# Kernel optimization log

Measured on AMD Instinct MI355X. Metric: run time of the kernel, lower is better.

Reference implementation:

```python
import jax, jax.numpy as jnp
import numpy as np

B, N, T, D, H, K = 16, 64, 32, 512, 256, 13
S = N * T  # flattened document length
PAD_TAG = 0


def setup_inputs():
    key = jax.random.key(0)
    ks = jax.random.split(key, 16)
    x = jax.random.normal(ks[0], (B, N, T, D), jnp.float32)
    x_gcn = jax.random.normal(ks[1], (B, N, D), jnp.float32)
    length = jax.random.randint(ks[2], (B, N), 1, T + 1)
    mask = (jnp.arange(T)[None, None, :] < length[:, :, None]).astype(jnp.int32)
    tags = jax.random.randint(ks[3], (B, N, T), 0, K)
    s = 0.05
    w_ih_f = jax.random.normal(ks[4], (4 * H, D), jnp.float32) * s
    w_hh_f = jax.random.normal(ks[5], (4 * H, H), jnp.float32) * s
    b_f = jax.random.normal(ks[6], (4 * H,), jnp.float32) * s
    w_ih_b = jax.random.normal(ks[7], (4 * H, D), jnp.float32) * s
    w_hh_b = jax.random.normal(ks[8], (4 * H, H), jnp.float32) * s
    b_b = jax.random.normal(ks[9], (4 * H,), jnp.float32) * s
    mlp_w = jax.random.normal(ks[10], (K, 2 * H), jnp.float32) * s
    mlp_b = jax.random.normal(ks[11], (K,), jnp.float32) * s
    transitions = jax.random.normal(ks[12], (K, K), jnp.float32) * s
    start_trans = jax.random.normal(ks[13], (K,), jnp.float32) * s
    end_trans = jax.random.normal(ks[14], (K,), jnp.float32) * s
    return dict(x=x, x_gcn=x_gcn, mask=mask, length=length, tags=tags,
                w_ih_f=w_ih_f, w_hh_f=w_hh_f, b_f=b_f,
                w_ih_b=w_ih_b, w_hh_b=w_hh_b, b_b=b_b,
                mlp_w=mlp_w, mlp_b=mlp_b,
                transitions=transitions, start_trans=start_trans, end_trans=end_trans)


def _pack_one(v, dest):
    # scatter valid rows to compacted positions; invalid rows land in dummy slot S
    out = jnp.zeros((S + 1,) + v.shape[1:], v.dtype).at[dest].set(v)
    return out[:S]


def union_layer(x, x_gcn, mask, length, tags):
    xf = x.reshape(B, S, D)
    mf = mask.reshape(B, S)
    tf = tags.reshape(B, S)
    doc_len = length.sum(-1)  # (B,)
    cum = jnp.cumsum(mf, axis=1)
    dest = jnp.where(mf == 1, cum - 1, S)  # invalid -> dummy slot
    new_x = jax.vmap(_pack_one)(xf, dest)
    new_tag = jax.vmap(_pack_one)(tf, dest)  # pad tag = 0
    new_mask = (jnp.arange(S)[None, :] < doc_len[:, None]).astype(mf.dtype)
    gcn_flat = jnp.broadcast_to(x_gcn[:, :, None, :], (B, N, T, D)).reshape(B, S, D)
    return gcn_flat + new_x, new_mask, doc_len, new_tag


def lstm_dir(xs, w_ih, w_hh, b):
    # xs: (B, S, Din) -> hidden states (B, S, H)
    def step(carry, xt):
        h, c = carry
        g = xt @ w_ih.T + h @ w_hh.T + b
        i, f, gg, o = jnp.split(g, 4, axis=-1)
        c = jax.nn.sigmoid(f) * c + jax.nn.sigmoid(i) * jnp.tanh(gg)
        h = jax.nn.sigmoid(o) * jnp.tanh(c)
        return (h, c), h
    init = (jnp.zeros((B, H), xs.dtype), jnp.zeros((B, H), xs.dtype))
    _, hs = jax.lax.scan(step, init, jnp.swapaxes(xs, 0, 1))
    return jnp.swapaxes(hs, 0, 1)


def bilstm(new_x, doc_len, w_ih_f, w_hh_f, b_f, w_ih_b, w_hh_b, b_b):
    t = jnp.arange(S)[None, :]
    L = doc_len[:, None]
    rev = jnp.where(t < L, L - 1 - t, t)  # per-sample reversal within valid region (involution)
    out_f = lstm_dir(new_x, w_ih_f, w_hh_f, b_f)
    x_rev = jnp.take_along_axis(new_x, rev[:, :, None], axis=1)
    out_b = lstm_dir(x_rev, w_ih_b, w_hh_b, b_b)
    out_b = jnp.take_along_axis(out_b, rev[:, :, None], axis=1)
    return jnp.concatenate([out_f, out_b], axis=-1)  # (B, S, 2H)


def crf_log_likelihood(logits, tags, mask, doc_len, transitions, start_trans, end_trans):
    maskf = mask.astype(logits.dtype)
    # numerator: score of the gold path
    emit = jnp.take_along_axis(logits, tags[:, :, None], axis=2)[..., 0]  # (B,S)
    num = start_trans[tags[:, 0]] + (emit * maskf).sum(1)
    tr = transitions[tags[:, :-1], tags[:, 1:]] * maskf[:, 1:]
    num = num + tr.sum(1)
    last_tag = jnp.take_along_axis(tags, (doc_len - 1)[:, None], axis=1)[:, 0]
    num = num + end_trans[last_tag]
    # denominator: forward algorithm
    alpha0 = start_trans[None, :] + logits[:, 0]
    def step(alpha, inp):
        e, m = inp  # (B,K), (B,)
        new = jax.nn.logsumexp(alpha[:, :, None] + transitions[None] + e[:, None, :], axis=1)
        return jnp.where(m[:, None] > 0, new, alpha), None
    alpha, _ = jax.lax.scan(step, alpha0,
                            (jnp.swapaxes(logits[:, 1:], 0, 1), jnp.swapaxes(mask[:, 1:], 0, 1)))
    log_z = jax.nn.logsumexp(alpha + end_trans[None, :], axis=-1)
    return num - log_z  # (B,) per-doc log-likelihood (keepdim=True)


def reference(x, x_gcn, mask, length, tags,
              w_ih_f, w_hh_f, b_f, w_ih_b, w_hh_b, b_b,
              mlp_w, mlp_b, transitions, start_trans, end_trans):
    new_x, new_mask, doc_len, new_tag = union_layer(x, x_gcn, mask, length, tags)
    out = bilstm(new_x, doc_len, w_ih_f, w_hh_f, b_f, w_ih_b, w_hh_b, b_b)
    out = out * new_mask[:, :, None].astype(out.dtype)  # packed-seq padding semantics
    logits = out @ mlp_w.T + mlp_b  # (B, S, K)
    ll = crf_log_likelihood(logits, new_tag, new_mask, doc_len,
                            transitions, start_trans, end_trans)
    return logits, new_mask, ll
```

## Files before the change

### kernel.cpp

```cpp
#include <hip/hip_runtime.h>
#include <hip/hip_fp16.h>
#include <hip/hip_bf16.h>

#define B_ 16
#define N_ 64
#define T_ 32
#define D_ 512
#define H_ 256
#define K_ 13
#define S_ 2048
#define G4_ 1024

typedef float f32x4 __attribute__((ext_vector_type(4)));
typedef short s16x8 __attribute__((ext_vector_type(8)));
typedef int   i32x4 __attribute__((ext_vector_type(4)));

#define LOG2E 1.44269504f
#define INVQ  2.0505324e-5f
#define INVQ2 2.9582873e-5f

#define BAR() do { \
  asm volatile("s_waitcnt lgkmcnt(0)" ::: "memory"); \
  __builtin_amdgcn_s_barrier(); \
  __builtin_amdgcn_sched_barrier(0); \
} while (0)

__device__ __forceinline__ float sigm(float x){ return 1.0f/(1.0f+__expf(-x)); }
__device__ __forceinline__ float tanh_fast(float x){ return 1.0f - 2.0f/(1.0f+__expf(2.0f*x)); }

__device__ __forceinline__ float sigm2(float y){ return __builtin_amdgcn_rcpf(1.0f + exp2f(-y)); }
__device__ __forceinline__ float tanh2(float y){ return 1.0f - 2.0f*__builtin_amdgcn_rcpf(1.0f + exp2f(2.0f*y)); }

__global__ void k_prep(const int* __restrict__ length, int* __restrict__ cum, int* __restrict__ doc){
  const int b = threadIdx.x >> 6, n = threadIdx.x & 63;
  const int v = length[b*N_ + n];
  int x = v;
  #pragma unroll
  for (int d = 1; d < 64; d <<= 1){
    int y = __shfl_up(x, d);
    if (n >= d) x += y;
  }
  cum[b*N_ + n] = x - v;
  if (n == 63) doc[b] = x;
}

__global__ __launch_bounds__(256) void k_cast(const float* __restrict__ wf, const float* __restrict__ wb,
                       const float* __restrict__ hf, const float* __restrict__ hb,
                       ushort* __restrict__ wih, signed char* __restrict__ whh8){
  const int i = blockIdx.x*256 + threadIdx.x;
  if (i < 2*G4_*D_){
    const int dir = i / (G4_*D_); const int r = i % (G4_*D_);
    const float v = dir ? wb[r] : wf[r];
    ((__hip_bfloat16*)wih)[i] = __float2bfloat16(v);
  } else {
    const int j2 = i - 2*G4_*D_;
    if (j2 < 2*G4_*H_){
      const int dir = j2 >> 18; const int r = j2 & 262143;
      const float v = (dir ? hb : hf)[r];
      int q = (int)rintf(v * 384.0f);
      whh8[j2] = (signed char)min(127, max(-127, q));
    }
  }
}

__global__ __launch_bounds__(256) void k_srcmap(const int* __restrict__ length, const int* __restrict__ cum,
                         const int* __restrict__ tags, int* __restrict__ src, int* __restrict__ ntag){
  const int i = blockIdx.x*256 + threadIdx.x;
  const int b = i >> 11, nt = i & 2047, n = nt >> 5, t = nt & 31;
  if (t < length[b*N_ + n]){
    const int dest = cum[b*N_ + n] + t;
    src[b*S_ + dest] = nt;
    ntag[b*S_ + dest] = tags[i];
  }
}

__global__ __launch_bounds__(256) void k_newx(const float* __restrict__ x, const float* __restrict__ gcn,
                      const int* __restrict__ src, const int* __restrict__ doc,
                      ushort* __restrict__ nx, float* __restrict__ mask_out){
  const int r = blockIdx.x; const int b = r >> 11, s = r & 2047;
  const int L = doc[b];
  const int d = threadIdx.x*2;
  const float2 g2 = *(const float2*)&gcn[((size_t)(b*N_ + (s>>5)))*D_ + d];
  float v0 = g2.x, v1 = g2.y;
  if (s < L){
    const int nt = src[r];
    const float2 x2 = *(const float2*)&x[((size_t)(b*S_ + nt))*D_ + d];
    v0 += x2.x; v1 += x2.y;
  }
  __hip_bfloat16* o = (__hip_bfloat16*)nx + (size_t)r*D_ + d;
  o[0] = __float2bfloat16(v0); o[1] = __float2bfloat16(v1);
  if (threadIdx.x == 0) mask_out[r] = (s < L) ? 1.0f : 0.0f;
}

__global__ __launch_bounds__(256) void k_gemm(const ushort* __restrict__ A, const ushort* __restrict__ Bw,
    const float* __restrict__ bias_f, const float* __restrict__ bias_b,
    const int* __restrict__ doc, __half* __restrict__ pre){
  const int m0 = blockIdx.x*128, n0 = blockIdx.y*128;
  const int b = m0 >> 11, s0 = m0 & 2047;
  if (s0 >= doc[b]) return;
  __shared__ __align__(16) ushort la[128*40];
  __shared__ __align__(16) ushort lb[128*40];
  const int tid = threadIdx.x, lane = tid & 63, w = tid >> 6;
  const int wr = w >> 1, wc = w & 1;
  const int fr = lane & 15, fq = lane >> 4;
  f32x4 acc[4][4] = {};
  const int srow = tid >> 1;
  const int sko  = (tid & 1)*16;
  for (int kt = 0; kt < 16; ++kt){
    const int k0 = kt*32;
    const float4 a0 = *(const float4*)&A[(size_t)(m0+srow)*512 + k0 + sko];
    const float4 a1 = *(const float4*)&A[(size_t)(m0+srow)*512 + k0 + sko + 8];
    const float4 b0 = *(const float4*)&Bw[(size_t)(n0+srow)*512 + k0 + sko];
    const float4 b1 = *(const float4*)&Bw[(size_t)(n0+srow)*512 + k0 + sko + 8];
    *(float4*)&la[srow*40 + sko]     = a0;
    *(float4*)&la[srow*40 + sko + 8] = a1;
    *(float4*)&lb[srow*40 + sko]     = b0;
    *(float4*)&lb[srow*40 + sko + 8] = b1;
    __syncthreads();
    s16x8 af[4], bfr[4];
    #pragma unroll
    for (int mi=0; mi<4; ++mi) af[mi] = *(const s16x8*)&la[(wr*64+mi*16+fr)*40 + fq*8];
    #pragma unroll
    for (int ni=0; ni<4; ++ni) bfr[ni] = *(const s16x8*)&lb[(wc*64+ni*16+fr)*40 + fq*8];
    #pragma unroll
    for (int mi=0; mi<4; ++mi){
      #pragma unroll
      for (int ni=0; ni<4; ++ni){
        acc[mi][ni] = __builtin_amdgcn_mfma_f32_16x16x32_bf16(af[mi], bfr[ni], acc[mi][ni], 0, 0, 0);
      }
    }
    __syncthreads();
  }
  #pragma unroll
  for (int ni=0; ni<4; ++ni){
    const int n = n0 + wc*64 + ni*16 + fr;
    const float bv = (n < 1024) ? bias_f[n] : bias_b[n-1024];
    const int dir = n >> 10, g = (n >> 8) & 3, u = n & 255;
    const int col = dir*1024 + u*4 + g;
    #pragma unroll
    for (int mi=0; mi<4; ++mi){
      const int mb = m0 + wr*64 + mi*16 + fq*4;
      #pragma unroll
      for (int j=0; j<4; ++j)
        pre[(size_t)(mb+j)*2048 + col] = __float2half((acc[mi][ni][j] + bv)*LOG2E);
    }
  }
}

__global__ __launch_bounds__(512, 2) void k_recur12(
    const signed char* __restrict__ W8,
    const __half* __restrict__ pre, const int* __restrict__ doc,
    __half* __restrict__ outh)
{
  const int b = blockIdx.x >> 1, dir = blockIdx.x & 1;
  const int tid = threadIdx.x, lane = tid & 63, wv = tid >> 6;
  const int L = doc[b];

  __shared__ __align__(16) signed char hq[2][256];

  if (tid < 128) ((unsigned*)hq)[tid] = 0u;

  i32x4 wfrag[2][4][4];
  #pragma unroll
  for (int nt = 0; nt < 2; ++nt)
    #pragma unroll
    for (int g = 0; g < 4; ++g){
      const int row = g*256 + wv*32 + nt*16 + (lane & 15);
      #pragma unroll
      for (int kt = 0; kt < 4; ++kt)
        wfrag[nt][g][kt] = *(const i32x4*)&W8[(size_t)dir*262144 + (size_t)row*256 + kt*64 + (lane>>4)*16];
    }

  const int u = wv*32 + (lane & 31);
  const int koff = (lane >> 4)*16;
  const int pos0 = dir ? (L-1) : 0;
  const __half* pp = pre + ((size_t)(b*S_ + pos0))*2048 + dir*1024 + u*4;
  __half*       op = outh + ((size_t)(b*S_ + pos0))*512 + dir*256 + u;
  const ptrdiff_t dp  = dir ? -2048 : 2048;
  const ptrdiff_t dph = dir ? -512  : 512;

  float cst = 0.f;
  uint2 pv, pvn = {0,0};
  pv = *(const uint2*)pp;
  const i32x4 z = {0,0,0,0};
  BAR();

  for (int t = 0; t < L; ++t){
    if (t+1 < L) pvn = *(const uint2*)(pp + dp);
    pp += dp;

    const int rbuf = (t+1) & 1, wbuf = t & 1;

    i32x4 af[4];
    #pragma unroll
    for (int kt = 0; kt < 4; ++kt)
      af[kt] = *(const i32x4*)&hq[rbuf][kt*64 + koff];

    auto chain4 = [&](const i32x4* w4) -> int {
      i32x4 a = __builtin_amdgcn_mfma_i32_16x16x64_i8(af[0], w4[0], z, 0, 0, 0);
      a = __builtin_amdgcn_mfma_i32_16x16x64_i8(af[1], w4[1], a, 0, 0, 0);
      a = __builtin_amdgcn_mfma_i32_16x16x64_i8(af[2], w4[2], a, 0, 0, 0);
      a = __builtin_amdgcn_mfma_i32_16x16x64_i8(af[3], w4[3], a, 0, 0, 0);
      return a[0];
    };

    const bool hi = (lane & 16) != 0;
    const __half2* ph = (const __half2*)&pv;
    const float2 p01 = __half22float2(ph[0]);
    const float2 p23 = __half22float2(ph[1]);

    const int i0 = chain4(wfrag[0][0]), i1 = chain4(wfrag[1][0]);
    const int f0 = chain4(wfrag[0][1]), f1 = chain4(wfrag[1][1]);
    const int q0 = chain4(wfrag[0][2]), q1 = chain4(wfrag[1][2]);
    const float giy = (float)(hi ? i1 : i0)*INVQ2 + p01.x;
    const float gfy = (float)(hi ? f1 : f0)*INVQ2 + p01.y;
    const float ggy = (float)(hi ? q1 : q0)*INVQ2 + p23.x;
    const int o0 = chain4(wfrag[0][3]), o1 = chain4(wfrag[1][3]);
    const float c = sigm2(gfy)*cst + sigm2(giy)*tanh2(ggy);
    cst = c;
    const float goy = (float)(hi ? o1 : o0)*INVQ2 + p23.y;
    const float hval = sigm2(goy)*tanh2(c*LOG2E);

    if (lane < 32){
      *op = __float2half(hval);
      hq[wbuf][u] = (signed char)(int)rintf(hval*127.0f);
    }
    op += dph;
    pv = pvn;
    BAR();
  }
}

__global__ __launch_bounds__(256) void k_logits(const __half* __restrict__ outh, const float* __restrict__ mw,
    const float* __restrict__ mb, const int* __restrict__ doc, float* __restrict__ logits){
  const int w = threadIdx.x >> 6, lane = threadIdx.x & 63;
  const int r = blockIdx.x*4 + w;
  const int b = r >> 11, s = r & 2047;
  if (s >= doc[b]){
    if (lane < 13) logits[(size_t)r*13 + lane] = mb[lane];
    return;
  }
  float xv[8];
  #pragma unroll
  for (int m=0; m<8; ++m) xv[m] = __half2float(outh[(size_t)r*512 + lane + m*64]);
  #pragma unroll
  for (int k=0; k<13; ++k){
    float p = 0.f;
    #pragma unroll
    for (int m=0; m<8; ++m) p += xv[m]*mw[k*512 + lane + m*64];
    #pragma unroll
    for (int off=32; off; off>>=1) p += __shfl_down(p, off);
    if (lane == 0) logits[(size_t)r*13 + k] = p + mb[k];
  }
}

__global__ void k_crf(const float* __restrict__ logits, const int* __restrict__ ntag,
    const int* __restrict__ doc, const float* __restrict__ trans,
    const float* __restrict__ stt, const float* __restrict__ ent, float* __restrict__ ll){
  const int b = blockIdx.x, lane = threadIdx.x;
  const int L = doc[b];
  const float* lg = logits + (size_t)b*S_*13;
  float et[13];
  #pragma unroll
  for (int i=0; i<13; ++i) et[i] = (lane < 13) ? __expf(trans[i*13 + lane]) : 0.f;
  float alpha = (lane < 13) ? (stt[lane] + lg[lane]) : -1e30f;
  float e_nxt = (L > 1 && lane < 13) ? lg[13 + lane] : 0.f;
  for (int t=1; t<L; ++t){
    const float e = e_nxt;
    if (t+1 < L && lane < 13) e_nxt = lg[(size_t)(t+1)*13 + lane];
    float m = alpha;
    #pragma unroll
    for (int off = 1; off < 16; off <<= 1) m = fmaxf(m, __shfl_xor(m, off));
    const float a = __expf(alpha - m);
    float s = 0.f;
    #pragma unroll
    for (int i=0; i<13; ++i) s += __shfl(a, i) * et[i];
    alpha = m + __logf(s) + e;
  }
  float av = (lane < 13) ? alpha + ent[lane] : -1e30f;
  float m2 = -1e30f;
  #pragma unroll
  for (int i=0; i<13; ++i) m2 = fmaxf(m2, __shfl(av, i));
  float s2 = 0.f;
  #pragma unroll
  for (int i=0; i<13; ++i) s2 += __expf(__shfl(av, i) - m2);
  const float logz = m2 + __logf(s2);
  const int* tg = ntag + (size_t)b*S_;
  float num = 0.f;
  for (int t = lane; t < L; t += 64){
    const int cur = tg[t];
    num += lg[(size_t)t*13 + cur];
    if (t >= 1) num += trans[tg[t-1]*13 + cur];
  }
  #pragma unroll
  for (int off=32; off; off>>=1) num += __shfl_down(num, off);
  if (lane == 0){
    num += stt[tg[0]] + ent[tg[L-1]];
    ll[b] = num - logz;
  }
}

extern "C" void kernel_launch(void* const* d_in, const int* in_sizes, int n_in,
                              void* d_out, int out_size, void* d_ws, size_t ws_size,
                              hipStream_t stream){
  const float* x    = (const float*)d_in[0];
  const float* gcn  = (const float*)d_in[1];
  const int* length = (const int*)d_in[3];
  const int* tags   = (const int*)d_in[4];
  const float* wihf = (const float*)d_in[5];
  const float* whhf = (const float*)d_in[6];
  const float* bf   = (const float*)d_in[7];
  const float* wihb = (const float*)d_in[8];
  const float* whhb = (const float*)d_in[9];
  const float* bb   = (const float*)d_in[10];
  const float* mw   = (const float*)d_in[11];
  const float* mb   = (const float*)d_in[12];
  const float* trans= (const float*)d_in[13];
  const float* stt  = (const float*)d_in[14];
  const float* ent  = (const float*)d_in[15];

  char* ws = (char*)d_ws;
  ushort* nx   = (ushort*)(ws + 0);
  __half* pre  = (__half*)(ws + 33554432);
  __half* outh = (__half*)(ws + 167772160);
  ushort* wih  = (ushort*)(ws + 234881024);
  signed char* whh8 = (signed char*)(ws + 236978176);
  int*    src  = (int*)(ws + 238026752);
  int*    ntag = (int*)(ws + 238157824);
  int*    cum  = (int*)(ws + 238288896);
  int*    doc  = (int*)(ws + 238292992);

  float* logits  = (float*)d_out;
  float* maskout = logits + 425984;
  float* ll      = maskout + 32768;

  hipLaunchKernelGGL(k_prep,   dim3(1),        dim3(1024), 0, stream, length, cum, doc);
  hipLaunchKernelGGL(k_cast,   dim3(6144),     dim3(256),  0, stream, wihf, wihb, whhf, whhb, wih, whh8);
  hipLaunchKernelGGL(k_srcmap, dim3(128),      dim3(256),  0, stream, length, cum, tags, src, ntag);
  hipLaunchKernelGGL(k_newx,   dim3(32768),    dim3(256),  0, stream, x, gcn, src, doc, nx, maskout);
  hipLaunchKernelGGL(k_gemm,   dim3(256, 16),  dim3(256),  0, stream, nx, wih, bf, bb, doc, pre);
  hipLaunchKernelGGL(k_recur12, dim3(32),      dim3(512),  0, stream, whh8, pre, doc, outh);
  hipLaunchKernelGGL(k_logits, dim3(8192),     dim3(256),  0, stream, outh, mw, mb, doc, logits);
  hipLaunchKernelGGL(k_crf,    dim3(16),       dim3(64),   0, stream, logits, ntag, doc, trans, stt, ent, ll);
}
```

Measured before the change: 1.535 ms.

## Compute MLP logits with fp16 MFMA and streamline CRF forward in log2 domain

The per-row wave-reduction logits kernel becomes an MFMA 16x16x32 fp16 kernel, with the MLP weights pre-cast to half in k_prep and staged in shared memory. The output buffer is memset to zero so padded rows produce bias-only logits without a per-row length check. The CRF forward pass moves to base-2 exp/log and uses a tree-shaped sum. This adds a 32 MB memset, and the MLP weights are rounded to fp16.

```diff
diff --git a/kernel.cpp b/kernel.cpp
--- a/kernel.cpp
+++ b/kernel.cpp
@@ -14,6 +14,7 @@
 typedef float f32x4 __attribute__((ext_vector_type(4)));
 typedef short s16x8 __attribute__((ext_vector_type(8)));
 typedef int   i32x4 __attribute__((ext_vector_type(4)));
+typedef _Float16 f16x8 __attribute__((ext_vector_type(8)));
 
 #define LOG2E 1.44269504f
 #define INVQ  2.0505324e-5f
@@ -25,13 +26,11 @@
   __builtin_amdgcn_sched_barrier(0); \
 } while (0)
 
-__device__ __forceinline__ float sigm(float x){ return 1.0f/(1.0f+__expf(-x)); }
-__device__ __forceinline__ float tanh_fast(float x){ return 1.0f - 2.0f/(1.0f+__expf(2.0f*x)); }
-
 __device__ __forceinline__ float sigm2(float y){ return __builtin_amdgcn_rcpf(1.0f + exp2f(-y)); }
 __device__ __forceinline__ float tanh2(float y){ return 1.0f - 2.0f*__builtin_amdgcn_rcpf(1.0f + exp2f(2.0f*y)); }
 
-__global__ void k_prep(const int* __restrict__ length, int* __restrict__ cum, int* __restrict__ doc){
+__global__ void k_prep(const int* __restrict__ length, int* __restrict__ cum, int* __restrict__ doc,
+                       const float* __restrict__ mw, __half* __restrict__ mwh){
   const int b = threadIdx.x >> 6, n = threadIdx.x & 63;
   const int v = length[b*N_ + n];
   int x = v;
@@ -42,6 +41,11 @@
   }
   cum[b*N_ + n] = x - v;
   if (n == 63) doc[b] = x;
+  #pragma unroll
+  for (int k = 0; k < 8; ++k){
+    const int i = threadIdx.x + k*1024;
+    mwh[i] = (i < 13*512) ? __float2half(mw[i]) : __float2half(0.0f);
+  }
 }
 
 __global__ __launch_bounds__(256) void k_cast(const float* __restrict__ wf, const float* __restrict__ wb,
@@ -147,7 +151,7 @@
   }
 }
 
-__global__ __launch_bounds__(512, 2) void k_recur12(
+__global__ __launch_bounds__(512, 2) void k_recur16(
     const signed char* __restrict__ W8,
     const __half* __restrict__ pre, const int* __restrict__ doc,
     __half* __restrict__ outh)
@@ -231,26 +235,33 @@
   }
 }
 
-__global__ __launch_bounds__(256) void k_logits(const __half* __restrict__ outh, const float* __restrict__ mw,
-    const float* __restrict__ mb, const int* __restrict__ doc, float* __restrict__ logits){
-  const int w = threadIdx.x >> 6, lane = threadIdx.x & 63;
-  const int r = blockIdx.x*4 + w;
-  const int b = r >> 11, s = r & 2047;
-  if (s >= doc[b]){
-    if (lane < 13) logits[(size_t)r*13 + lane] = mb[lane];
-    return;
-  }
-  float xv[8];
-  #pragma unroll
-  for (int m=0; m<8; ++m) xv[m] = __half2float(outh[(size_t)r*512 + lane + m*64]);
-  #pragma unroll
-  for (int k=0; k<13; ++k){
-    float p = 0.f;
-    #pragma unroll
-    for (int m=0; m<8; ++m) p += xv[m]*mw[k*512 + lane + m*64];
-    #pragma unroll
-    for (int off=32; off; off>>=1) p += __shfl_down(p, off);
-    if (lane == 0) logits[(size_t)r*13 + k] = p + mb[k];
+__global__ __launch_bounds__(256) void k_logits(const __half* __restrict__ outh, const __half* __restrict__ mwh,
+    const float* __restrict__ mb, float* __restrict__ logits){
+  __shared__ __align__(16) __half lw[16][520];
+  const int tid = threadIdx.x, lane = tid & 63, wv = tid >> 6;
+  {
+    const int i = tid*8;
+    #pragma unroll
+    for (int k = 0; k < 4; ++k){
+      const int ii = i + k*2048;
+      *(uint4*)&lw[ii >> 9][ii & 511] = *(const uint4*)&mwh[ii];
+    }
+  }
+  __syncthreads();
+  const int fr = lane & 15, fq = lane >> 4;
+  const int row0 = blockIdx.x*64 + wv*16;
+  f32x4 acc = {0.f, 0.f, 0.f, 0.f};
+  #pragma unroll
+  for (int kt = 0; kt < 16; ++kt){
+    const f16x8 a  = *(const f16x8*)&outh[(size_t)(row0 + fr)*512 + kt*32 + fq*8];
+    const f16x8 bf = *(const f16x8*)&lw[fr][kt*32 + fq*8];
+    acc = __builtin_amdgcn_mfma_f32_16x16x32_f16(a, bf, acc, 0, 0, 0);
+  }
+  if (fr < 13){
+    const float bv = mb[fr];
+    #pragma unroll
+    for (int j = 0; j < 4; ++j)
+      logits[(size_t)(row0 + fq*4 + j)*13 + fr] = acc[j] + bv;
   }
 }
 
@@ -260,31 +271,33 @@
   const int b = blockIdx.x, lane = threadIdx.x;
   const int L = doc[b];
   const float* lg = logits + (size_t)b*S_*13;
-  float et[13];
-  #pragma unroll
-  for (int i=0; i<13; ++i) et[i] = (lane < 13) ? __expf(trans[i*13 + lane]) : 0.f;
-  float alpha = (lane < 13) ? (stt[lane] + lg[lane]) : -1e30f;
-  float e_nxt = (L > 1 && lane < 13) ? lg[13 + lane] : 0.f;
+  float et2[13];
+  #pragma unroll
+  for (int i=0; i<13; ++i) et2[i] = (lane < 13) ? exp2f(trans[i*13 + lane]*LOG2E) : 0.f;
+  float al = (lane < 13) ? (stt[lane] + lg[lane])*LOG2E : -1e30f;
+  float e_nxt = (L > 1 && lane < 13) ? lg[13 + lane]*LOG2E : 0.f;
   for (int t=1; t<L; ++t){
     const float e = e_nxt;
-    if (t+1 < L && lane < 13) e_nxt = lg[(size_t)(t+1)*13 + lane];
-    float m = alpha;
+    if (t+1 < L && lane < 13) e_nxt = lg[(size_t)(t+1)*13 + lane]*LOG2E;
+    float m = al;
     #pragma unroll
     for (int off = 1; off < 16; off <<= 1) m = fmaxf(m, __shfl_xor(m, off));
-    const float a = __expf(alpha - m);
-    float s = 0.f;
-    #pragma unroll
-    for (int i=0; i<13; ++i) s += __shfl(a, i) * et[i];
-    alpha = m + __logf(s) + e;
-  }
-  float av = (lane < 13) ? alpha + ent[lane] : -1e30f;
+    const float a = exp2f(al - m);
+    float tv[13];
+    #pragma unroll
+    for (int i=0; i<13; ++i) tv[i] = __shfl(a, i) * et2[i];
+    const float s = (((tv[0]+tv[1])+(tv[2]+tv[3])) + ((tv[4]+tv[5])+(tv[6]+tv[7])))
+                  + (((tv[8]+tv[9])+(tv[10]+tv[11])) + tv[12]);
+    al = m + log2f(s) + e;
+  }
+  float av = (lane < 13) ? al + ent[lane]*LOG2E : -1e30f;
   float m2 = -1e30f;
   #pragma unroll
   for (int i=0; i<13; ++i) m2 = fmaxf(m2, __shfl(av, i));
   float s2 = 0.f;
   #pragma unroll
-  for (int i=0; i<13; ++i) s2 += __expf(__shfl(av, i) - m2);
-  const float logz = m2 + __logf(s2);
+  for (int i=0; i<13; ++i) s2 += exp2f(__shfl(av, i) - m2);
+  const float logz = (m2 + log2f(s2)) * (1.0f/LOG2E);
   const int* tg = ntag + (size_t)b*S_;
   float num = 0.f;
   for (int t = lane; t < L; t += 64){
@@ -325,6 +338,7 @@
   __half* outh = (__half*)(ws + 167772160);
   ushort* wih  = (ushort*)(ws + 234881024);
   signed char* whh8 = (signed char*)(ws + 236978176);
+  __half* mwh  = (__half*)(ws + 237502464);
   int*    src  = (int*)(ws + 238026752);
   int*    ntag = (int*)(ws + 238157824);
   int*    cum  = (int*)(ws + 238288896);
@@ -334,12 +348,13 @@
   float* maskout = logits + 425984;
   float* ll      = maskout + 32768;
 
-  hipLaunchKernelGGL(k_prep,   dim3(1),        dim3(1024), 0, stream, length, cum, doc);
+  hipLaunchKernelGGL(k_prep,   dim3(1),        dim3(1024), 0, stream, length, cum, doc, mw, mwh);
   hipLaunchKernelGGL(k_cast,   dim3(6144),     dim3(256),  0, stream, wihf, wihb, whhf, whhb, wih, whh8);
   hipLaunchKernelGGL(k_srcmap, dim3(128),      dim3(256),  0, stream, length, cum, tags, src, ntag);
   hipLaunchKernelGGL(k_newx,   dim3(32768),    dim3(256),  0, stream, x, gcn, src, doc, nx, maskout);
+  hipMemsetAsync(outh, 0, 33554432, stream);
   hipLaunchKernelGGL(k_gemm,   dim3(256, 16),  dim3(256),  0, stream, nx, wih, bf, bb, doc, pre);
-  hipLaunchKernelGGL(k_recur12, dim3(32),      dim3(512),  0, stream, whh8, pre, doc, outh);
-  hipLaunchKernelGGL(k_logits, dim3(8192),     dim3(256),  0, stream, outh, mw, mb, doc, logits);
+  hipLaunchKernelGGL(k_recur16, dim3(32),      dim3(512),  0, stream, whh8, pre, doc, outh);
+  hipLaunchKernelGGL(k_logits, dim3(512),      dim3(256),  0, stream, outh, mwh, mb, logits);
   hipLaunchKernelGGL(k_crf,    dim3(16),       dim3(64),   0, stream, logits, ntag, doc, trans, stt, ent, ll);
 }
```

After: 1.665 ms. 8.5% more time.
